# Performance work log

Hardware: AMD Instinct MI355X
Metric: run time of the kernel (lower is better)

The kernel has to match this reference:

```python
import jax, jax.numpy as jnp
import numpy as np

H = 16  # num attention heads
D = 1024  # hidden size
F = 4096  # intermediate size
LN_EPS = 1e-5


def _glorot(key, shape):
    fan_in, fan_out = shape[0], shape[1]
    lim = np.sqrt(6.0 / (fan_in + fan_out))
    return jax.random.uniform(key, shape, jnp.float32, -lim, lim)


def setup_inputs() -> dict:
    key = jax.random.key(0)
    ks = jax.random.split(key, 16)
    inp = {
        'input_tensor': jax.random.normal(ks[0], (4, 1024, D), jnp.float32),
        'ctx_tensor': jax.random.normal(ks[1], (4, 2048, D), jnp.float32),
        'ctx_attn_mask': jnp.zeros((4, 1, 1, 2048), jnp.float32),
        # cross-attention QKV
        'cq_w': _glorot(ks[2], (D, D)), 'cq_b': jnp.zeros((D,)),
        'ck_w': _glorot(ks[3], (D, D)), 'ck_b': jnp.zeros((D,)),
        'cv_w': _glorot(ks[4], (D, D)), 'cv_b': jnp.zeros((D,)),
        # cross output (dense + LN)
        'co_w': _glorot(ks[5], (D, D)), 'co_b': jnp.zeros((D,)),
        'co_g': jnp.ones((D,)), 'co_be': jnp.zeros((D,)),
        # self-attention QKV
        'sq_w': _glorot(ks[6], (D, D)), 'sq_b': jnp.zeros((D,)),
        'sk_w': _glorot(ks[7], (D, D)), 'sk_b': jnp.zeros((D,)),
        'sv_w': _glorot(ks[8], (D, D)), 'sv_b': jnp.zeros((D,)),
        # self-attention output
        'so_w': _glorot(ks[9], (D, D)), 'so_b': jnp.zeros((D,)),
        'so_g': jnp.ones((D,)), 'so_be': jnp.zeros((D,)),
        # FFN intermediate + output
        'fi_w': _glorot(ks[10], (D, F)), 'fi_b': jnp.zeros((F,)),
        'fo_w': _glorot(ks[11], (F, D)), 'fo_b': jnp.zeros((D,)),
        'fo_g': jnp.ones((D,)), 'fo_be': jnp.zeros((D,)),
    }
    return inp


def _split_heads(x):
    b, l, _ = x.shape
    return x.reshape(b, l, H, D // H)


def _mha(x, ctx, mask, qw, qb, kw, kb, vw, vb):
    # manual QK^T/sqrt(d) -> +mask -> softmax -> V (dropout=0 / eval)
    q = _split_heads(x @ qw + qb)       # [b, lq, h, d]
    k = _split_heads(ctx @ kw + kb)     # [b, lk, h, d]
    v = _split_heads(ctx @ vw + vb)
    scores = jnp.einsum('bqhd,bkhd->bhqk', q, k) / np.sqrt(D // H).astype(np.float32)
    if mask is not None:
        scores = scores + mask
    probs = jax.nn.softmax(scores, axis=-1)
    out = jnp.einsum('bhqk,bkhd->bqhd', probs, v)
    return out.reshape(x.shape[0], x.shape[1], D)


def _self_output(h, residual, w, b, g, be):
    h = h @ w + b
    h = h + residual
    mu = jnp.mean(h, axis=-1, keepdims=True)
    var = jnp.mean(jnp.square(h - mu), axis=-1, keepdims=True)
    return (h - mu) * jax.lax.rsqrt(var + LN_EPS) * g + be


def reference(input_tensor, ctx_tensor, ctx_attn_mask,
              cq_w, cq_b, ck_w, ck_b, cv_w, cv_b, co_w, co_b, co_g, co_be,
              sq_w, sq_b, sk_w, sk_b, sv_w, sv_b, so_w, so_b, so_g, so_be,
              fi_w, fi_b, fo_w, fo_b, fo_g, fo_be):
    # CrossLayer.forward
    ca = _mha(input_tensor, ctx_tensor, ctx_attn_mask, cq_w, cq_b, ck_w, ck_b, cv_w, cv_b)
    x = _self_output(ca, input_tensor, co_w, co_b, co_g, co_be)
    sa = _mha(x, x, None, sq_w, sq_b, sk_w, sk_b, sv_w, sv_b)
    x = _self_output(sa, x, so_w, so_b, so_g, so_be)
    inter = jax.nn.gelu(x @ fi_w + fi_b, approximate=False)
    x = _self_output(inter, x, fo_w, fo_b, fo_g, fo_be)
    return x
```

## Files before the change

kernel.cpp:

```cpp
#include <hip/hip_runtime.h>
#include <math.h>

typedef unsigned short ushort_t;
typedef __bf16 bf16x8 __attribute__((ext_vector_type(8)));
typedef float f32x4 __attribute__((ext_vector_type(4)));

__device__ __forceinline__ float bf2f(unsigned int u) {
    union { unsigned int i; float f; } v; v.i = u << 16; return v.f;
}
__device__ __forceinline__ ushort_t f2bf(float f) {
    union { float f; unsigned int i; } v; v.f = f;
    unsigned int u = v.i;
    unsigned int r = u + 0x7fffu + ((u >> 16) & 1u);
    return (ushort_t)(r >> 16);
}

__device__ __forceinline__ void gload16(const ushort_t* g, ushort_t* l) {
    __builtin_amdgcn_global_load_lds(
        (__attribute__((address_space(1))) void*)g,
        (__attribute__((address_space(3))) void*)l, 16, 0, 0);
}

__global__ void __launch_bounds__(256) cvt_bf16_kernel(
    const float* __restrict__ in, ushort_t* __restrict__ out, int n8)
{
    int i = blockIdx.x * 256 + threadIdx.x;
    if (i >= n8) return;
    size_t off = (size_t)i * 8;
    float4 a = *(const float4*)(in + off);
    float4 b = *(const float4*)(in + off + 4);
    ushort_t o[8] = {f2bf(a.x), f2bf(a.y), f2bf(a.z), f2bf(a.w),
                     f2bf(b.x), f2bf(b.y), f2bf(b.z), f2bf(b.w)};
    *(uint4*)(out + off) = *(const uint4*)o;
}

__global__ void __launch_bounds__(256) wconv_kernel(
    const float* __restrict__ W, ushort_t* __restrict__ Wt, int K, int N)
{
    __shared__ float tile[32][33];
    const int t = threadIdx.x;
    const int k0 = blockIdx.x * 32, n0 = blockIdx.y * 32;
    const int r = t >> 3, c4 = (t & 7) * 4;
    float4 d = *(const float4*)(&W[(size_t)(k0 + r) * N + n0 + c4]);
    tile[r][c4 + 0] = d.x; tile[r][c4 + 1] = d.y;
    tile[r][c4 + 2] = d.z; tile[r][c4 + 3] = d.w;
    __syncthreads();
    ushort_t o[4] = { f2bf(tile[c4 + 0][r]), f2bf(tile[c4 + 1][r]),
                      f2bf(tile[c4 + 2][r]), f2bf(tile[c4 + 3][r]) };
    *(uint2*)(&Wt[(size_t)(n0 + r) * K + k0 + c4]) = *(const uint2*)o;
}

#define BM 128
#define BN 128
#define BK 32

template <int MODE>
__global__ void __launch_bounds__(256) gemm_bt_kernel(
    const ushort_t* __restrict__ A,
    const ushort_t* __restrict__ B0, const ushort_t* __restrict__ B1,
    const ushort_t* __restrict__ B2,
    const float* __restrict__ bias0, const float* __restrict__ bias1,
    const float* __restrict__ bias2,
    ushort_t* __restrict__ C0, ushort_t* __restrict__ C1,
    ushort_t* __restrict__ C2,
    int M, int N, int K)
{
    __shared__ __align__(16) ushort_t As[2][BM * BK];
    __shared__ __align__(16) ushort_t Bs[2][BN * BK];

    const int z = blockIdx.z;
    const ushort_t* Bt = (z == 0) ? B0 : ((z == 1) ? B1 : B2);
    const float* bias = (z == 0) ? bias0 : ((z == 1) ? bias1 : bias2);
    ushort_t* Cout = (z == 0) ? C0 : ((z == 1) ? C1 : C2);

    const int tid = threadIdx.x;
    const int m0 = blockIdx.y * BM, n0 = blockIdx.x * BN;
    const int wave = tid >> 6, lane = tid & 63;
    const int wm = wave >> 1, wn = wave & 1;
    const int lr = lane & 15;
    const int lk = (lane >> 4) * 8;

    const ushort_t* Ab = A + (size_t)m0 * K;
    const ushort_t* Bb = Bt + (size_t)n0 * K;
    const int srow = tid >> 2;
    const int sc8 = (tid & 3) * 8;

    f32x4 acc[4][4];
#pragma unroll
    for (int i = 0; i < 4; i++)
#pragma unroll
        for (int j = 0; j < 4; j++) acc[i][j] = (f32x4){0.f, 0.f, 0.f, 0.f};

    const int nt = K / BK;

    {
        const size_t ga = (size_t)srow * K + sc8;
        gload16(Ab + ga,                 &As[0][tid * 8]);
        gload16(Ab + ga + (size_t)64 * K, &As[0][2048 + tid * 8]);
        gload16(Bb + ga,                 &Bs[0][tid * 8]);
        gload16(Bb + ga + (size_t)64 * K, &Bs[0][2048 + tid * 8]);
    }
    asm volatile("s_waitcnt vmcnt(0)" ::: "memory");
    __syncthreads();

    int cur = 0;
    for (int t = 0; t < nt; ++t) {
        if (t + 1 < nt) {
            const size_t ga = (size_t)srow * K + (size_t)(t + 1) * BK + sc8;
            gload16(Ab + ga,                 &As[cur ^ 1][tid * 8]);
            gload16(Ab + ga + (size_t)64 * K, &As[cur ^ 1][2048 + tid * 8]);
            gload16(Bb + ga,                 &Bs[cur ^ 1][tid * 8]);
            gload16(Bb + ga + (size_t)64 * K, &Bs[cur ^ 1][2048 + tid * 8]);
        }
        bf16x8 af[4], bfr[4];
#pragma unroll
        for (int i = 0; i < 4; i++)
            af[i] = *(const bf16x8*)(&As[cur][(wm * 64 + i * 16 + lr) * BK + lk]);
#pragma unroll
        for (int j = 0; j < 4; j++)
            bfr[j] = *(const bf16x8*)(&Bs[cur][(wn * 64 + j * 16 + lr) * BK + lk]);
#pragma unroll
        for (int i = 0; i < 4; i++)
#pragma unroll
            for (int j = 0; j < 4; j++)
                acc[i][j] = __builtin_amdgcn_mfma_f32_16x16x32_bf16(af[i], bfr[j], acc[i][j], 0, 0, 0);
        asm volatile("s_waitcnt vmcnt(0)" ::: "memory");
        __syncthreads();
        cur ^= 1;
    }

    const int rq = (lane >> 4) * 4;
#pragma unroll
    for (int j = 0; j < 4; j++) {
        const int col = n0 + wn * 64 + j * 16 + lr;
        const float bv = bias[col];
#pragma unroll
        for (int i = 0; i < 4; i++) {
#pragma unroll
            for (int r = 0; r < 4; r++) {
                const int row = m0 + wm * 64 + i * 16 + rq + r;
                float v = acc[i][j][r] + bv;
                if (MODE == 2) {
                    v = 0.5f * v * (1.0f + erff(v * 0.70710678118654752f));
                }
                Cout[(size_t)row * N + col] = f2bf(v);
            }
        }
    }
}

__global__ void __launch_bounds__(256) mfma_attn_kernel(
    const ushort_t* __restrict__ Q, const ushort_t* __restrict__ Kt,
    const ushort_t* __restrict__ Vt, const float* __restrict__ mask,
    ushort_t* __restrict__ O, int Lq, int Lk, float scale)
{
    __shared__ __align__(16) ushort_t qs[64][72];
    __shared__ __align__(16) ushort_t ks[32][72];
    __shared__ __align__(16) ushort_t vsT[64][40];
    __shared__ __align__(16) ushort_t ps[4][16][40];

    const int tid = threadIdx.x;
    const int wave = tid >> 6, lane = tid & 63;
    const int quad = lane >> 4, lc = lane & 15;
    const int b = blockIdx.y >> 4, h = blockIdx.y & 15;
    const int q0 = blockIdx.x * 64;
    const size_t qbase = ((size_t)b * Lq) * 1024 + h * 64;
    const size_t kbase = ((size_t)b * Lk) * 1024 + h * 64;

#pragma unroll
    for (int r = 0; r < 2; r++) {
        int v = r * 256 + tid;
        int row = v >> 3, c8 = (v & 7) * 8;
        *(uint4*)(&qs[row][c8]) = *(const uint4*)(&Q[qbase + (size_t)(q0 + row) * 1024 + c8]);
    }
    __syncthreads();

    bf16x8 qa0 = *(const bf16x8*)(&qs[wave * 16 + lc][quad * 8]);
    bf16x8 qa1 = *(const bf16x8*)(&qs[wave * 16 + lc][32 + quad * 8]);

    f32x4 o[4];
#pragma unroll
    for (int d = 0; d < 4; d++) o[d] = (f32x4){0.f, 0.f, 0.f, 0.f};
    float m_i[4], l_i[4];
#pragma unroll
    for (int r = 0; r < 4; r++) { m_i[r] = -1e30f; l_i[r] = 0.f; }

    for (int kt = 0; kt < Lk; kt += 32) {
        __syncthreads();
        {
            int row = tid >> 3, c8 = (tid & 7) * 8;
            const size_t gk = kbase + (size_t)(kt + row) * 1024 + c8;
            *(uint4*)(&ks[row][c8]) = *(const uint4*)(&Kt[gk]);
            uint4 vv = *(const uint4*)(&Vt[gk]);
            const ushort_t* vp = (const ushort_t*)&vv;
#pragma unroll
            for (int i = 0; i < 8; i++) {
                int d = c8 + i;
                vsT[d][row ^ (((d >> 3) & 3) << 3)] = vp[i];
            }
        }
        __syncthreads();

        bf16x8 kb00 = *(const bf16x8*)(&ks[lc][quad * 8]);
        bf16x8 kb01 = *(const bf16x8*)(&ks[lc][32 + quad * 8]);
        bf16x8 kb10 = *(const bf16x8*)(&ks[16 + lc][quad * 8]);
        bf16x8 kb11 = *(const bf16x8*)(&ks[16 + lc][32 + quad * 8]);
        f32x4 s0 = (f32x4){0.f, 0.f, 0.f, 0.f};
        f32x4 s1 = (f32x4){0.f, 0.f, 0.f, 0.f};
        s0 = __builtin_amdgcn_mfma_f32_16x16x32_bf16(qa0, kb00, s0, 0, 0, 0);
        s0 = __builtin_amdgcn_mfma_f32_16x16x32_bf16(qa1, kb01, s0, 0, 0, 0);
        s1 = __builtin_amdgcn_mfma_f32_16x16x32_bf16(qa0, kb10, s1, 0, 0, 0);
        s1 = __builtin_amdgcn_mfma_f32_16x16x32_bf16(qa1, kb11, s1, 0, 0, 0);

        float mk0 = mask ? mask[(size_t)b * Lk + kt + lc] : 0.f;
        float mk1 = mask ? mask[(size_t)b * Lk + kt + 16 + lc] : 0.f;

        float alpha[4];
#pragma unroll
        for (int r = 0; r < 4; r++) {
            float v0 = s0[r] * scale + mk0;
            float v1 = s1[r] * scale + mk1;
            float mx = fmaxf(v0, v1);
#pragma unroll
            for (int off = 1; off < 16; off <<= 1) mx = fmaxf(mx, __shfl_xor(mx, off, 64));
            float mnew = fmaxf(m_i[r], mx);
            alpha[r] = __expf(m_i[r] - mnew);
            m_i[r] = mnew;
            float p0 = __expf(v0 - mnew);
            float p1 = __expf(v1 - mnew);
            ps[wave][quad * 4 + r][lc] = f2bf(p0);
            ps[wave][quad * 4 + r][16 + lc] = f2bf(p1);
            float psum = p0 + p1;
#pragma unroll
            for (int off = 1; off < 16; off <<= 1) psum += __shfl_xor(psum, off, 64);
            l_i[r] = l_i[r] * alpha[r] + psum;
        }
#pragma unroll
        for (int d = 0; d < 4; d++)
#pragma unroll
            for (int r = 0; r < 4; r++) o[d][r] *= alpha[r];

        bf16x8 pa = *(const bf16x8*)(&ps[wave][lc][quad * 8]);
#pragma unroll
        for (int d = 0; d < 4; d++) {
            int dr = d * 16 + lc;
            bf16x8 vb = *(const bf16x8*)(&vsT[dr][(quad * 8) ^ ((((dr) >> 3) & 3) << 3)]);
            o[d] = __builtin_amdgcn_mfma_f32_16x16x32_bf16(pa, vb, o[d], 0, 0, 0);
        }
    }

#pragma unroll
    for (int d = 0; d < 4; d++) {
#pragma unroll
        for (int r = 0; r < 4; r++) {
            float val = o[d][r] / l_i[r];
            O[qbase + (size_t)(q0 + wave * 16 + quad * 4 + r) * 1024 + d * 16 + lc] = f2bf(val);
        }
    }
}

template <bool RES_F32, bool OUT_F32>
__global__ void __launch_bounds__(256) ln_kernel(
    const ushort_t* __restrict__ Hbuf, const void* __restrict__ Res,
    const float* __restrict__ gamma, const float* __restrict__ beta,
    void* __restrict__ Out)
{
    const int row = blockIdx.x;
    const int tid = threadIdx.x;
    const size_t base = (size_t)row * 1024 + tid * 4;

    uint2 hh = *(const uint2*)(Hbuf + base);
    float v[4];
    v[0] = bf2f(hh.x & 0xffffu);
    v[1] = bf2f(hh.x >> 16);
    v[2] = bf2f(hh.y & 0xffffu);
    v[3] = bf2f(hh.y >> 16);
    if (RES_F32) {
        float4 rv = *(const float4*)((const float*)Res + base);
        v[0] += rv.x; v[1] += rv.y; v[2] += rv.z; v[3] += rv.w;
    } else {
        uint2 rr = *(const uint2*)((const ushort_t*)Res + base);
        v[0] += bf2f(rr.x & 0xffffu);
        v[1] += bf2f(rr.x >> 16);
        v[2] += bf2f(rr.y & 0xffffu);
        v[3] += bf2f(rr.y >> 16);
    }

    float s = v[0] + v[1] + v[2] + v[3];
    float s2 = v[0]*v[0] + v[1]*v[1] + v[2]*v[2] + v[3]*v[3];
#pragma unroll
    for (int o = 1; o < 64; o <<= 1) {
        s += __shfl_xor(s, o, 64);
        s2 += __shfl_xor(s2, o, 64);
    }
    __shared__ float red[8];
    const int wv = tid >> 6, ln_ = tid & 63;
    if (ln_ == 0) { red[wv] = s; red[wv + 4] = s2; }
    __syncthreads();
    s = red[0] + red[1] + red[2] + red[3];
    s2 = red[4] + red[5] + red[6] + red[7];
    const float mu = s * (1.0f / 1024.0f);
    const float var = s2 * (1.0f / 1024.0f) - mu * mu;
    const float rstd = rsqrtf(var + 1e-5f);

    float4 gv = *(const float4*)(&gamma[tid * 4]);
    float4 bv = *(const float4*)(&beta[tid * 4]);
    float o0 = (v[0] - mu) * rstd * gv.x + bv.x;
    float o1 = (v[1] - mu) * rstd * gv.y + bv.y;
    float o2 = (v[2] - mu) * rstd * gv.z + bv.z;
    float o3 = (v[3] - mu) * rstd * gv.w + bv.w;

    if (OUT_F32) {
        float4 of = {o0, o1, o2, o3};
        *(float4*)((float*)Out + base) = of;
    } else {
        ushort_t ob[4] = {f2bf(o0), f2bf(o1), f2bf(o2), f2bf(o3)};
        *(uint2*)((ushort_t*)Out + base) = *(uint2*)ob;
    }
}

extern "C" void kernel_launch(void* const* d_in, const int* in_sizes, int n_in,
                              void* d_out, int out_size, void* d_ws, size_t ws_size,
                              hipStream_t stream)
{
    const float* input = (const float*)d_in[0];
    const float* ctx   = (const float*)d_in[1];
    const float* mask  = (const float*)d_in[2];
    const float* cq_w = (const float*)d_in[3],  *cq_b = (const float*)d_in[4];
    const float* ck_w = (const float*)d_in[5],  *ck_b = (const float*)d_in[6];
    const float* cv_w = (const float*)d_in[7],  *cv_b = (const float*)d_in[8];
    const float* co_w = (const float*)d_in[9],  *co_b = (const float*)d_in[10];
    const float* co_g = (const float*)d_in[11], *co_be = (const float*)d_in[12];
    const float* sq_w = (const float*)d_in[13], *sq_b = (const float*)d_in[14];
    const float* sk_w = (const float*)d_in[15], *sk_b = (const float*)d_in[16];
    const float* sv_w = (const float*)d_in[17], *sv_b = (const float*)d_in[18];
    const float* so_w = (const float*)d_in[19], *so_b = (const float*)d_in[20];
    const float* so_g = (const float*)d_in[21], *so_be = (const float*)d_in[22];
    const float* fi_w = (const float*)d_in[23], *fi_b = (const float*)d_in[24];
    const float* fo_w = (const float*)d_in[25], *fo_b = (const float*)d_in[26];
    const float* fo_g = (const float*)d_in[27], *fo_be = (const float*)d_in[28];

    char* p = (char*)d_ws;
    const size_t MB = 1024 * 1024;
    ushort_t* Bq   = (ushort_t*)(p + 0 * MB);
    ushort_t* Bk   = (ushort_t*)(p + 8 * MB);
    ushort_t* Bv   = (ushort_t*)(p + 24 * MB);
    ushort_t* Ba   = (ushort_t*)(p + 40 * MB);
    ushort_t* Bh   = (ushort_t*)(p + 48 * MB);
    ushort_t* Bx1  = (ushort_t*)(p + 56 * MB);
    ushort_t* Bx2  = (ushort_t*)(p + 64 * MB);
    ushort_t* Bi   = Bk;
    ushort_t* Xctx = Ba;
    ushort_t* Xin  = Bx2;
    ushort_t* WtA  = (ushort_t*)(p + 56 * MB);
    ushort_t* WtB  = (ushort_t*)(p + 58 * MB);
    ushort_t* WtC  = (ushort_t*)(p + 60 * MB);
    ushort_t* WtD  = (ushort_t*)(p + 64 * MB);
    ushort_t* WtE  = (ushort_t*)(p + 66 * MB);
    ushort_t* WtF  = (ushort_t*)(p + 68 * MB);
    ushort_t* WtG  = (ushort_t*)(p + 0 * MB);

    const float scale = 0.125f;
    dim3 blk(256);

    cvt_bf16_kernel<<<2048, blk, 0, stream>>>(input, Xin, 524288);
    cvt_bf16_kernel<<<4096, blk, 0, stream>>>(ctx, Xctx, 1048576);

    wconv_kernel<<<dim3(32, 32), blk, 0, stream>>>(cq_w, WtA, 1024, 1024);
    wconv_kernel<<<dim3(32, 32), blk, 0, stream>>>(ck_w, WtB, 1024, 1024);
    wconv_kernel<<<dim3(32, 32), blk, 0, stream>>>(cv_w, WtC, 1024, 1024);
    gemm_bt_kernel<0><<<dim3(8, 32, 1), blk, 0, stream>>>(
        Xin, WtA, WtA, WtA, cq_b, cq_b, cq_b, Bq, Bq, Bq, 4096, 1024, 1024);
    gemm_bt_kernel<0><<<dim3(8, 64, 2), blk, 0, stream>>>(
        Xctx, WtB, WtC, WtC, ck_b, cv_b, cv_b, Bk, Bv, Bv, 8192, 1024, 1024);
    mfma_attn_kernel<<<dim3(16, 64), blk, 0, stream>>>(Bq, Bk, Bv, mask, Ba, 1024, 2048, scale);
    wconv_kernel<<<dim3(32, 32), blk, 0, stream>>>(co_w, WtA, 1024, 1024);
    gemm_bt_kernel<0><<<dim3(8, 32, 1), blk, 0, stream>>>(
        Ba, WtA, WtA, WtA, co_b, co_b, co_b, Bh, Bh, Bh, 4096, 1024, 1024);
    ln_kernel<true, false><<<dim3(4096), blk, 0, stream>>>(Bh, input, co_g, co_be, Bx1);

    wconv_kernel<<<dim3(32, 32), blk, 0, stream>>>(sq_w, WtD, 1024, 1024);
    wconv_kernel<<<dim3(32, 32), blk, 0, stream>>>(sk_w, WtE, 1024, 1024);
    wconv_kernel<<<dim3(32, 32), blk, 0, stream>>>(sv_w, WtF, 1024, 1024);
    gemm_bt_kernel<0><<<dim3(8, 32, 3), blk, 0, stream>>>(
        Bx1, WtD, WtE, WtF, sq_b, sk_b, sv_b, Bq, Bk, Bv, 4096, 1024, 1024);
    mfma_attn_kernel<<<dim3(16, 64), blk, 0, stream>>>(Bq, Bk, Bv, nullptr, Ba, 1024, 1024, scale);
    wconv_kernel<<<dim3(32, 32), blk, 0, stream>>>(so_w, WtD, 1024, 1024);
    gemm_bt_kernel<0><<<dim3(8, 32, 1), blk, 0, stream>>>(
        Ba, WtD, WtD, WtD, so_b, so_b, so_b, Bh, Bh, Bh, 4096, 1024, 1024);
    ln_kernel<false, false><<<dim3(4096), blk, 0, stream>>>(Bh, Bx1, so_g, so_be, Bx2);

    wconv_kernel<<<dim3(32, 128), blk, 0, stream>>>(fi_w, WtG, 1024, 4096);
    gemm_bt_kernel<2><<<dim3(32, 32, 1), blk, 0, stream>>>(
        Bx2, WtG, WtG, WtG, fi_b, fi_b, fi_b, Bi, Bi, Bi, 4096, 4096, 1024);
    wconv_kernel<<<dim3(128, 32), blk, 0, stream>>>(fo_w, WtG, 4096, 1024);
    gemm_bt_kernel<0><<<dim3(8, 32, 1), blk, 0, stream>>>(
        Bi, WtG, WtG, WtG, fo_b, fo_b, fo_b, Bh, Bh, Bh, 4096, 1024, 4096);
    ln_kernel<false, true><<<dim3(4096), blk, 0, stream>>>(Bh, Bx2, fo_g, fo_be, (float*)d_out);
}
```

Baseline: 804.0 us.

## Narrow GEMM N-tile for small-N GEMMs and widen attention KV tiles with prefetch

The GEMM kernel is templated on the N tile width, and the N=1024 GEMMs now use 64-wide tiles so more blocks are launched across the CUs. The FFN-up GEMM keeps 128-wide tiles. The attention kernel processes 64 keys per iteration instead of 32 and prefetches the next K/V tile into registers while the current tile is being stored. It also remaps block IDs so that blocks sharing a batch and head are grouped, and raises wave priority around the MFMA sections. These changes cost more LDS and registers in attention and give less A-tile reuse per block in the GEMMs.

```diff
diff --git a/kernel.cpp b/kernel.cpp
--- a/kernel.cpp
+++ b/kernel.cpp
@@ -51,10 +51,9 @@
 }
 
 #define BM 128
-#define BN 128
 #define BK 32
 
-template <int MODE>
+template <int MODE, int BNT>
 __global__ void __launch_bounds__(256) gemm_bt_kernel(
     const ushort_t* __restrict__ A,
     const ushort_t* __restrict__ B0, const ushort_t* __restrict__ B1,
@@ -66,7 +65,10 @@
     int M, int N, int K)
 {
     __shared__ __align__(16) ushort_t As[2][BM * BK];
-    __shared__ __align__(16) ushort_t Bs[2][BN * BK];
+    __shared__ __align__(16) ushort_t Bs[2][BNT * BK];
+
+    constexpr int NJ = BNT / 32;
+    constexpr int WN = BNT / 2;
 
     const int z = blockIdx.z;
     const ushort_t* Bt = (z == 0) ? B0 : ((z == 1) ? B1 : B2);
@@ -74,7 +76,7 @@
     ushort_t* Cout = (z == 0) ? C0 : ((z == 1) ? C1 : C2);
 
     const int tid = threadIdx.x;
-    const int m0 = blockIdx.y * BM, n0 = blockIdx.x * BN;
+    const int m0 = blockIdx.y * BM, n0 = blockIdx.x * BNT;
     const int wave = tid >> 6, lane = tid & 63;
     const int wm = wave >> 1, wn = wave & 1;
     const int lr = lane & 15;
@@ -85,20 +87,21 @@
     const int srow = tid >> 2;
     const int sc8 = (tid & 3) * 8;
 
-    f32x4 acc[4][4];
+    f32x4 acc[4][NJ];
 #pragma unroll
     for (int i = 0; i < 4; i++)
 #pragma unroll
-        for (int j = 0; j < 4; j++) acc[i][j] = (f32x4){0.f, 0.f, 0.f, 0.f};
+        for (int j = 0; j < NJ; j++) acc[i][j] = (f32x4){0.f, 0.f, 0.f, 0.f};
 
     const int nt = K / BK;
 
     {
         const size_t ga = (size_t)srow * K + sc8;
-        gload16(Ab + ga,                 &As[0][tid * 8]);
+        gload16(Ab + ga,                  &As[0][tid * 8]);
         gload16(Ab + ga + (size_t)64 * K, &As[0][2048 + tid * 8]);
-        gload16(Bb + ga,                 &Bs[0][tid * 8]);
-        gload16(Bb + ga + (size_t)64 * K, &Bs[0][2048 + tid * 8]);
+        gload16(Bb + ga,                  &Bs[0][tid * 8]);
+        if (BNT == 128)
+            gload16(Bb + ga + (size_t)64 * K, &Bs[0][2048 + tid * 8]);
     }
     asm volatile("s_waitcnt vmcnt(0)" ::: "memory");
     __syncthreads();
@@ -107,22 +110,23 @@
     for (int t = 0; t < nt; ++t) {
         if (t + 1 < nt) {
             const size_t ga = (size_t)srow * K + (size_t)(t + 1) * BK + sc8;
-            gload16(Ab + ga,                 &As[cur ^ 1][tid * 8]);
+            gload16(Ab + ga,                  &As[cur ^ 1][tid * 8]);
             gload16(Ab + ga + (size_t)64 * K, &As[cur ^ 1][2048 + tid * 8]);
-            gload16(Bb + ga,                 &Bs[cur ^ 1][tid * 8]);
-            gload16(Bb + ga + (size_t)64 * K, &Bs[cur ^ 1][2048 + tid * 8]);
-        }
-        bf16x8 af[4], bfr[4];
+            gload16(Bb + ga,                  &Bs[cur ^ 1][tid * 8]);
+            if (BNT == 128)
+                gload16(Bb + ga + (size_t)64 * K, &Bs[cur ^ 1][2048 + tid * 8]);
+        }
+        bf16x8 af[4], bfr[NJ];
 #pragma unroll
         for (int i = 0; i < 4; i++)
             af[i] = *(const bf16x8*)(&As[cur][(wm * 64 + i * 16 + lr) * BK + lk]);
 #pragma unroll
-        for (int j = 0; j < 4; j++)
-            bfr[j] = *(const bf16x8*)(&Bs[cur][(wn * 64 + j * 16 + lr) * BK + lk]);
+        for (int j = 0; j < NJ; j++)
+            bfr[j] = *(const bf16x8*)(&Bs[cur][(wn * WN + j * 16 + lr) * BK + lk]);
 #pragma unroll
         for (int i = 0; i < 4; i++)
 #pragma unroll
-            for (int j = 0; j < 4; j++)
+            for (int j = 0; j < NJ; j++)
                 acc[i][j] = __builtin_amdgcn_mfma_f32_16x16x32_bf16(af[i], bfr[j], acc[i][j], 0, 0, 0);
         asm volatile("s_waitcnt vmcnt(0)" ::: "memory");
         __syncthreads();
@@ -131,8 +135,8 @@
 
     const int rq = (lane >> 4) * 4;
 #pragma unroll
-    for (int j = 0; j < 4; j++) {
-        const int col = n0 + wn * 64 + j * 16 + lr;
+    for (int j = 0; j < NJ; j++) {
+        const int col = n0 + wn * WN + j * 16 + lr;
         const float bv = bias[col];
 #pragma unroll
         for (int i = 0; i < 4; i++) {
@@ -155,17 +159,22 @@
     ushort_t* __restrict__ O, int Lq, int Lk, float scale)
 {
     __shared__ __align__(16) ushort_t qs[64][72];
-    __shared__ __align__(16) ushort_t ks[32][72];
-    __shared__ __align__(16) ushort_t vsT[64][40];
-    __shared__ __align__(16) ushort_t ps[4][16][40];
+    __shared__ __align__(16) ushort_t ks[64][72];
+    __shared__ __align__(16) ushort_t vsT[64][72];
+    __shared__ __align__(16) ushort_t ps[4][16][72];
 
     const int tid = threadIdx.x;
     const int wave = tid >> 6, lane = tid & 63;
     const int quad = lane >> 4, lc = lane & 15;
-    const int b = blockIdx.y >> 4, h = blockIdx.y & 15;
-    const int q0 = blockIdx.x * 64;
+
+    const int id = blockIdx.x + (int)gridDim.x * blockIdx.y;
+    const int bh = (id & 7) * 8 + ((id >> 3) >> 4);
+    const int qt = (id >> 3) & 15;
+    const int b = bh >> 4, h = bh & 15;
+    const int q0 = qt * 64;
     const size_t qbase = ((size_t)b * Lq) * 1024 + h * 64;
     const size_t kbase = ((size_t)b * Lk) * 1024 + h * 64;
+    const float* maskb = mask ? (mask + (size_t)b * Lk) : nullptr;
 
 #pragma unroll
     for (int r = 0; r < 2; r++) {
@@ -185,42 +194,67 @@
 #pragma unroll
     for (int r = 0; r < 4; r++) { m_i[r] = -1e30f; l_i[r] = 0.f; }
 
-    for (int kt = 0; kt < Lk; kt += 32) {
+    const int sr = tid >> 2;
+    const int d0c = (tid & 3) * 16;
+    const int vswz = (tid & 3) << 3;
+    const int vcol = sr ^ vswz;
+
+    const int nt = Lk >> 6;
+    size_t gk = kbase + (size_t)sr * 1024 + d0c;
+
+    uint4 kA = *(const uint4*)(Kt + gk);
+    uint4 kB = *(const uint4*)(Kt + gk + 8);
+    uint4 vA = *(const uint4*)(Vt + gk);
+    uint4 vB = *(const uint4*)(Vt + gk + 8);
+
+    for (int t = 0; t < nt; ++t) {
+        const int kt = t << 6;
         __syncthreads();
+        *(uint4*)(&ks[sr][d0c])     = kA;
+        *(uint4*)(&ks[sr][d0c + 8]) = kB;
         {
-            int row = tid >> 3, c8 = (tid & 7) * 8;
-            const size_t gk = kbase + (size_t)(kt + row) * 1024 + c8;
-            *(uint4*)(&ks[row][c8]) = *(const uint4*)(&Kt[gk]);
-            uint4 vv = *(const uint4*)(&Vt[gk]);
-            const ushort_t* vp = (const ushort_t*)&vv;
-#pragma unroll
-            for (int i = 0; i < 8; i++) {
-                int d = c8 + i;
-                vsT[d][row ^ (((d >> 3) & 3) << 3)] = vp[i];
-            }
+            const ushort_t* vp = (const ushort_t*)&vA;
+            const ushort_t* wp = (const ushort_t*)&vB;
+#pragma unroll
+            for (int i = 0; i < 8; i++) vsT[d0c + i][vcol]     = vp[i];
+#pragma unroll
+            for (int i = 0; i < 8; i++) vsT[d0c + 8 + i][vcol] = wp[i];
+        }
+        if (t + 1 < nt) {
+            gk += 64 * 1024;
+            kA = *(const uint4*)(Kt + gk);
+            kB = *(const uint4*)(Kt + gk + 8);
+            vA = *(const uint4*)(Vt + gk);
+            vB = *(const uint4*)(Vt + gk + 8);
         }
         __syncthreads();
 
-        bf16x8 kb00 = *(const bf16x8*)(&ks[lc][quad * 8]);
-        bf16x8 kb01 = *(const bf16x8*)(&ks[lc][32 + quad * 8]);
-        bf16x8 kb10 = *(const bf16x8*)(&ks[16 + lc][quad * 8]);
-        bf16x8 kb11 = *(const bf16x8*)(&ks[16 + lc][32 + quad * 8]);
-        f32x4 s0 = (f32x4){0.f, 0.f, 0.f, 0.f};
-        f32x4 s1 = (f32x4){0.f, 0.f, 0.f, 0.f};
-        s0 = __builtin_amdgcn_mfma_f32_16x16x32_bf16(qa0, kb00, s0, 0, 0, 0);
-        s0 = __builtin_amdgcn_mfma_f32_16x16x32_bf16(qa1, kb01, s0, 0, 0, 0);
-        s1 = __builtin_amdgcn_mfma_f32_16x16x32_bf16(qa0, kb10, s1, 0, 0, 0);
-        s1 = __builtin_amdgcn_mfma_f32_16x16x32_bf16(qa1, kb11, s1, 0, 0, 0);
-
-        float mk0 = mask ? mask[(size_t)b * Lk + kt + lc] : 0.f;
-        float mk1 = mask ? mask[(size_t)b * Lk + kt + 16 + lc] : 0.f;
+        float mk[4];
+#pragma unroll
+        for (int g = 0; g < 4; g++)
+            mk[g] = maskb ? maskb[kt + g * 16 + lc] : 0.f;
+
+        f32x4 s[4];
+        __builtin_amdgcn_s_setprio(1);
+#pragma unroll
+        for (int g = 0; g < 4; g++) {
+            bf16x8 k0 = *(const bf16x8*)(&ks[g * 16 + lc][quad * 8]);
+            bf16x8 k1 = *(const bf16x8*)(&ks[g * 16 + lc][32 + quad * 8]);
+            f32x4 z = (f32x4){0.f, 0.f, 0.f, 0.f};
+            z = __builtin_amdgcn_mfma_f32_16x16x32_bf16(qa0, k0, z, 0, 0, 0);
+            z = __builtin_amdgcn_mfma_f32_16x16x32_bf16(qa1, k1, z, 0, 0, 0);
+            s[g] = z;
+        }
+        __builtin_amdgcn_s_setprio(0);
 
         float alpha[4];
 #pragma unroll
         for (int r = 0; r < 4; r++) {
-            float v0 = s0[r] * scale + mk0;
-            float v1 = s1[r] * scale + mk1;
-            float mx = fmaxf(v0, v1);
+            float v0 = s[0][r] * scale + mk[0];
+            float v1 = s[1][r] * scale + mk[1];
+            float v2 = s[2][r] * scale + mk[2];
+            float v3 = s[3][r] * scale + mk[3];
+            float mx = fmaxf(fmaxf(v0, v1), fmaxf(v2, v3));
 #pragma unroll
             for (int off = 1; off < 16; off <<= 1) mx = fmaxf(mx, __shfl_xor(mx, off, 64));
             float mnew = fmaxf(m_i[r], mx);
@@ -228,9 +262,13 @@
             m_i[r] = mnew;
             float p0 = __expf(v0 - mnew);
             float p1 = __expf(v1 - mnew);
-            ps[wave][quad * 4 + r][lc] = f2bf(p0);
+            float p2 = __expf(v2 - mnew);
+            float p3 = __expf(v3 - mnew);
+            ps[wave][quad * 4 + r][lc]      = f2bf(p0);
             ps[wave][quad * 4 + r][16 + lc] = f2bf(p1);
-            float psum = p0 + p1;
+            ps[wave][quad * 4 + r][32 + lc] = f2bf(p2);
+            ps[wave][quad * 4 + r][48 + lc] = f2bf(p3);
+            float psum = (p0 + p1) + (p2 + p3);
 #pragma unroll
             for (int off = 1; off < 16; off <<= 1) psum += __shfl_xor(psum, off, 64);
             l_i[r] = l_i[r] * alpha[r] + psum;
@@ -240,13 +278,18 @@
 #pragma unroll
             for (int r = 0; r < 4; r++) o[d][r] *= alpha[r];
 
-        bf16x8 pa = *(const bf16x8*)(&ps[wave][lc][quad * 8]);
-#pragma unroll
-        for (int d = 0; d < 4; d++) {
-            int dr = d * 16 + lc;
-            bf16x8 vb = *(const bf16x8*)(&vsT[dr][(quad * 8) ^ ((((dr) >> 3) & 3) << 3)]);
-            o[d] = __builtin_amdgcn_mfma_f32_16x16x32_bf16(pa, vb, o[d], 0, 0, 0);
-        }
+        __builtin_amdgcn_s_setprio(1);
+#pragma unroll
+        for (int kk = 0; kk < 2; kk++) {
+            bf16x8 pa = *(const bf16x8*)(&ps[wave][lc][kk * 32 + quad * 8]);
+#pragma unroll
+            for (int d = 0; d < 4; d++) {
+                int dr = d * 16 + lc;
+                bf16x8 vb = *(const bf16x8*)(&vsT[dr][(kk * 32 + quad * 8) ^ (d << 3)]);
+                o[d] = __builtin_amdgcn_mfma_f32_16x16x32_bf16(pa, vb, o[d], 0, 0, 0);
+            }
+        }
+        __builtin_amdgcn_s_setprio(0);
     }
 
 #pragma unroll
@@ -369,32 +412,32 @@
     wconv_kernel<<<dim3(32, 32), blk, 0, stream>>>(cq_w, WtA, 1024, 1024);
     wconv_kernel<<<dim3(32, 32), blk, 0, stream>>>(ck_w, WtB, 1024, 1024);
     wconv_kernel<<<dim3(32, 32), blk, 0, stream>>>(cv_w, WtC, 1024, 1024);
-    gemm_bt_kernel<0><<<dim3(8, 32, 1), blk, 0, stream>>>(
+    gemm_bt_kernel<0, 64><<<dim3(16, 32, 1), blk, 0, stream>>>(
         Xin, WtA, WtA, WtA, cq_b, cq_b, cq_b, Bq, Bq, Bq, 4096, 1024, 1024);
-    gemm_bt_kernel<0><<<dim3(8, 64, 2), blk, 0, stream>>>(
+    gemm_bt_kernel<0, 64><<<dim3(16, 64, 2), blk, 0, stream>>>(
         Xctx, WtB, WtC, WtC, ck_b, cv_b, cv_b, Bk, Bv, Bv, 8192, 1024, 1024);
     mfma_attn_kernel<<<dim3(16, 64), blk, 0, stream>>>(Bq, Bk, Bv, mask, Ba, 1024, 2048, scale);
     wconv_kernel<<<dim3(32, 32), blk, 0, stream>>>(co_w, WtA, 1024, 1024);
-    gemm_bt_kernel<0><<<dim3(8, 32, 1), blk, 0, stream>>>(
+    gemm_bt_kernel<0, 64><<<dim3(16, 32, 1), blk, 0, stream>>>(
         Ba, WtA, WtA, WtA, co_b, co_b, co_b, Bh, Bh, Bh, 4096, 1024, 1024);
     ln_kernel<true, false><<<dim3(4096), blk, 0, stream>>>(Bh, input, co_g, co_be, Bx1);
 
     wconv_kernel<<<dim3(32, 32), blk, 0, stream>>>(sq_w, WtD, 1024, 1024);
     wconv_kernel<<<dim3(32, 32), blk, 0, stream>>>(sk_w, WtE, 1024, 1024);
     wconv_kernel<<<dim3(32, 32), blk, 0, stream>>>(sv_w, WtF, 1024, 1024);
-    gemm_bt_kernel<0><<<dim3(8, 32, 3), blk, 0, stream>>>(
+    gemm_bt_kernel<0, 64><<<dim3(16, 32, 3), blk, 0, stream>>>(
         Bx1, WtD, WtE, WtF, sq_b, sk_b, sv_b, Bq, Bk, Bv, 4096, 1024, 1024);
     mfma_attn_kernel<<<dim3(16, 64), blk, 0, stream>>>(Bq, Bk, Bv, nullptr, Ba, 1024, 1024, scale);
     wconv_kernel<<<dim3(32, 32), blk, 0, stream>>>(so_w, WtD, 1024, 1024);
-    gemm_bt_kernel<0><<<dim3(8, 32, 1), blk, 0, stream>>>(
+    gemm_bt_kernel<0, 64><<<dim3(16, 32, 1), blk, 0, stream>>>(
         Ba, WtD, WtD, WtD, so_b, so_b, so_b, Bh, Bh, Bh, 4096, 1024, 1024);
     ln_kernel<false, false><<<dim3(4096), blk, 0, stream>>>(Bh, Bx1, so_g, so_be, Bx2);
 
     wconv_kernel<<<dim3(32, 128), blk, 0, stream>>>(fi_w, WtG, 1024, 4096);
-    gemm_bt_kernel<2><<<dim3(32, 32, 1), blk, 0, stream>>>(
+    gemm_bt_kernel<2, 128><<<dim3(32, 32, 1), blk, 0, stream>>>(
         Bx2, WtG, WtG, WtG, fi_b, fi_b, fi_b, Bi, Bi, Bi, 4096, 4096, 1024);
     wconv_kernel<<<dim3(128, 32), blk, 0, stream>>>(fo_w, WtG, 4096, 1024);
-    gemm_bt_kernel<0><<<dim3(8, 32, 1), blk, 0, stream>>>(
+    gemm_bt_kernel<0, 64><<<dim3(16, 32, 1), blk, 0, stream>>>(
         Bi, WtG, WtG, WtG, fo_b, fo_b, fo_b, Bh, Bh, Bh, 4096, 1024, 4096);
     ln_kernel<false, true><<<dim3(4096), blk, 0, stream>>>(Bh, Bx2, fo_g, fo_be, (float*)d_out);
 }
```

Measured after the change: 718.8 us. -10.6%, faster.
